# Performance work log

Hardware: AMD Instinct MI355X
Metric: run time of the kernel (lower is better)

## Reference

```python
import math
import jax, jax.numpy as jnp
import numpy as np

DIM = 256; DEPTH = 5; FANOUT = 10; VOCAB = 257
B = 16; T = 2048
NEXP = 8; HID = 512; TOPK = 2; TEMP = 1.0; HEADS = 2
CAPACITY = math.ceil(B * TOPK / NEXP * 1.1)  # capacity-based dispatch, =5
LAYER_SIZES = [FANOUT ** l for l in range(DEPTH)]  # [1,10,100,1000,10000]


def setup_inputs() -> dict:
    key = jax.random.key(0)
    ks = iter(jax.random.split(key, 64))
    def p(shape, scale=0.02):
        return jax.random.normal(next(ks), shape, jnp.float32) * scale
    inp = {
        'tokens': jax.random.randint(next(ks), (B, T), 0, VOCAB),
        'embed': p((VOCAB, DIM)),
        'pin_w': p((DIM, DIM)), 'pin_b': jnp.zeros(DIM, jnp.float32),
        'pch_w': p((DIM, DIM)), 'pch_b': jnp.zeros(DIM, jnp.float32),
        'depth_bias': p((DEPTH, DIM)),
        'q_w': p((DIM, DIM)), 'q_b': jnp.zeros(DIM, jnp.float32),
        'k_w': p((DIM, DIM)), 'k_b': jnp.zeros(DIM, jnp.float32),
        'v_w': p((DIM, DIM)), 'v_b': jnp.zeros(DIM, jnp.float32),
        'o_w': p((DIM, DIM)), 'o_b': jnp.zeros(DIM, jnp.float32),
        'level_gate': jnp.zeros(DEPTH, jnp.float32),
        'depth_gate': jnp.zeros((DEPTH, DIM), jnp.float32),
        'in_proj_w': p((DIM, 3 * DIM)), 'in_proj_b': jnp.zeros(3 * DIM, jnp.float32),
        'out_proj_w': p((DIM, DIM)), 'out_proj_b': jnp.zeros(DIM, jnp.float32),
        'ln_g': jnp.ones(DIM, jnp.float32), 'ln_b': jnp.zeros(DIM, jnp.float32),
        'ic_gate': jnp.zeros(1, jnp.float32),
        'gate_w': p((DIM, NEXP)), 'gate_b': jnp.zeros(NEXP, jnp.float32),
        'ew1': p((NEXP, DIM, HID)), 'eb1': jnp.zeros((NEXP, HID), jnp.float32),
        'ew2': p((NEXP, HID, DIM)), 'eb2': jnp.zeros((NEXP, DIM), jnp.float32),
        'hw1': p((DIM, DIM)), 'hb1': jnp.zeros(DIM, jnp.float32),
        'hw2': p((DIM, VOCAB)), 'hb2': jnp.zeros(VOCAB, jnp.float32),
    }
    return inp


def _fractal(context, pin_w, pin_b, pch_w, pch_b, depth_bias, q_w, q_b, k_w, k_b,
             v_w, v_b, o_w, o_b, level_gate, depth_gate,
             in_proj_w, in_proj_b, out_proj_w, out_proj_b, ln_g, ln_b, ic_gate):
    Bc = context.shape[0]
    base = context @ pin_w + pin_b                       # [B,D]
    y_next = None
    level_means = [None] * DEPTH
    inv_sqrt_d = 1.0 / math.sqrt(DIM)
    for l in reversed(range(DEPTH)):
        n = LAYER_SIZES[l]
        if l == DEPTH - 1:
            child_agg = jnp.zeros((Bc, n, DIM), context.dtype)
        else:
            yg = y_next.reshape(Bc, n, FANOUT, DIM)      # children grouped per parent
            q = (base + depth_bias[l]) @ q_w + q_b       # [B,D], shared across nodes
            k = yg @ k_w + k_b
            v = yg @ v_w + v_b
            att = jax.nn.softmax(jnp.einsum('bd,bnfd->bnf', q, k) * inv_sqrt_d, axis=-1)
            child_agg = jax.nn.sigmoid(depth_gate[l]) * jnp.einsum('bnf,bnfd->bnd', att, v)
        gate = jax.nn.sigmoid(level_gate[l])
        upd = (base[:, None, :] + depth_bias[l][None, None, :] + child_agg @ pch_w + pch_b) * gate
        y = jax.nn.relu(upd) @ o_w + o_b                 # [B,n,D]
        level_means[l] = y.mean(axis=1)
        y_next = y
    root = y_next[:, 0, :]                               # n==1 at level 0
    # interconnect: MHA over per-level means [B,DEPTH,D]
    z = jnp.stack(level_means, axis=1)
    qkv = z @ in_proj_w + in_proj_b
    qh, kh, vh = jnp.split(qkv, 3, axis=-1)
    hd = DIM // HEADS
    def to_heads(t):
        return t.reshape(Bc, DEPTH, HEADS, hd).transpose(0, 2, 1, 3)
    qh, kh, vh = to_heads(qh), to_heads(kh), to_heads(vh)
    aw = jax.nn.softmax(jnp.einsum('bhqd,bhkd->bhqk', qh, kh) / math.sqrt(hd), axis=-1)
    z2 = jnp.einsum('bhqk,bhkd->bhqd', aw, vh).transpose(0, 2, 1, 3).reshape(Bc, DEPTH, DIM)
    z2 = z2 @ out_proj_w + out_proj_b
    zs = z + z2
    mu = zs.mean(-1, keepdims=True)
    var = ((zs - mu) ** 2).mean(-1, keepdims=True)
    zn = (zs - mu) / jnp.sqrt(var + 1e-5) * ln_g + ln_b
    return root + jax.nn.sigmoid(ic_gate) * zn[:, 0, :]


def _moe(ctx, gate_w, gate_b, ew1, eb1, ew2, eb2):
    scaled = (ctx @ gate_w + gate_b) / TEMP
    top_vals, top_idx = jax.lax.top_k(scaled, TOPK)      # [B,K]
    gs = jax.nn.softmax(top_vals, axis=-1)               # [B,K], strictly > 0
    out = jnp.zeros_like(ctx)
    for e in range(NEXP):                                # fixed small expert loop
        sflat = jnp.where(top_idx == e, gs, -1.0).reshape(-1)   # [B*K]
        vals, pos = jax.lax.top_k(sflat, CAPACITY)       # capacity-limited dispatch
        w = jnp.where(vals > 0.0, vals, 0.0)             # drop unassigned/overflow
        tok = pos // TOPK
        xin = ctx[tok]                                   # [cap,D]
        eo = jax.nn.relu(xin @ ew1[e] + eb1[e]) @ ew2[e] + eb2[e]
        out = out.at[tok].add(eo * w[:, None])
    return out


def reference(tokens, embed, pin_w, pin_b, pch_w, pch_b, depth_bias,
              q_w, q_b, k_w, k_b, v_w, v_b, o_w, o_b, level_gate, depth_gate,
              in_proj_w, in_proj_b, out_proj_w, out_proj_b, ln_g, ln_b, ic_gate,
              gate_w, gate_b, ew1, eb1, ew2, eb2, hw1, hb1, hw2, hb2):
    x = embed[tokens]                                    # [B,T,D]
    context = x.mean(axis=1)                             # [B,D]
    root = _fractal(context, pin_w, pin_b, pch_w, pch_b, depth_bias, q_w, q_b,
                    k_w, k_b, v_w, v_b, o_w, o_b, level_gate, depth_gate,
                    in_proj_w, in_proj_b, out_proj_w, out_proj_b, ln_g, ln_b, ic_gate)
    root = root + _moe(root, gate_w, gate_b, ew1, eb1, ew2, eb2)
    h = x + root[:, None, :]                             # per-token logits from context + token emb
    logits = jax.nn.relu(h @ hw1 + hb1) @ hw2 + hb2      # [B,T,V]
    return logits
```

## Files before the change

### kernel.cpp

```cpp
#include <hip/hip_runtime.h>
#include <hip/hip_bf16.h>
#include <math.h>

#define DIM    256
#define DEPTH  5
#define FANOUT 10
#define VOCAB  257
#define BB     16
#define TT     2048
#define NEXP   8
#define HID    512
#define TOPK   2
#define CAP    5

__device__ __forceinline__ float sigm(float x) { return 1.f / (1.f + expf(-x)); }

__device__ __forceinline__ void mv8x2(const float* sv, const float* __restrict__ W,
                                      int kseg, int cq, float red[16][DIM]) {
  const float* Wp = W + (size_t)kseg * 16 * DIM + cq * 4;
  float4 acc = {0.f, 0.f, 0.f, 0.f};
#pragma unroll 1
  for (int h = 0; h < 2; ++h) {
    float4 wv[8];
#pragma unroll
    for (int i = 0; i < 8; ++i)
      wv[i] = *(const float4*)(Wp + (size_t)(h * 8 + i) * DIM);
#pragma unroll
    for (int i = 0; i < 8; ++i) {
      float s = sv[kseg * 16 + h * 8 + i];
      acc.x = fmaf(s, wv[i].x, acc.x);
      acc.y = fmaf(s, wv[i].y, acc.y);
      acc.z = fmaf(s, wv[i].z, acc.z);
      acc.w = fmaf(s, wv[i].w, acc.w);
    }
    __builtin_amdgcn_sched_barrier(0);
  }
  *(float4*)&red[kseg][cq * 4] = acc;
}

__device__ __forceinline__ float sum16(const float red[16][DIM], int d) {
  float s = 0.f;
#pragma unroll
  for (int g = 0; g < 16; ++g) s += red[g][d];
  return s;
}

__global__ void __launch_bounds__(1024) k_fractal(
    const int* __restrict__ tokens, const float* __restrict__ embed,
    const float* __restrict__ pin_w, const float* __restrict__ pin_b,
    const float* __restrict__ pch_w, const float* __restrict__ pch_b,
    const float* __restrict__ depth_bias,
    const float* __restrict__ v_w, const float* __restrict__ v_b,
    const float* __restrict__ o_w, const float* __restrict__ o_b,
    const float* __restrict__ level_gate, const float* __restrict__ depth_gate,
    const float* __restrict__ in_proj_w, const float* __restrict__ in_proj_b,
    const float* __restrict__ out_proj_w, const float* __restrict__ out_proj_b,
    const float* __restrict__ ln_g, const float* __restrict__ ln_b,
    const float* __restrict__ ic_gate,
    float* __restrict__ rootA, float* __restrict__ root2,
    int* __restrict__ bidx, int* __restrict__ boff) {
  int b = blockIdx.x;
  int tid = threadIdx.x;
  int d = tid & 255;
  int ks = tid >> 8;
  int k0 = ks * 64;
  int kseg = tid >> 6;
  int cq = tid & 63;
  __shared__ int cnt[VOCAB];
  __shared__ float sv[DIM];
  __shared__ float basev[DIM];
  __shared__ float ym[DEPTH][DIM];
  __shared__ float q0v[DIM], kh[DEPTH][DIM], vh[DEPTH][DIM];
  __shared__ float red11[4][11][DIM];
  __shared__ float zsv[DIM];
  __shared__ float aw[16];
  __shared__ float redl[8];
  __shared__ int offb[VOCAB + 1];
  __shared__ int woff[VOCAB];
  float (*red16)[DIM] = reinterpret_cast<float(*)[DIM]>(&red11[0][0][0]);

  for (int i = tid; i < VOCAB; i += 1024) cnt[i] = 0;
  __syncthreads();
  for (int t = tid; t < TT; t += 1024) atomicAdd(&cnt[tokens[b * TT + t]], 1);
  __syncthreads();
  {
    const float* Ep = embed + (size_t)kseg * 16 * DIM + cq * 4;
    float4 acc = {0.f, 0.f, 0.f, 0.f};
#pragma unroll 1
    for (int h = 0; h < 2; ++h) {
      float4 ev[8];
#pragma unroll
      for (int i = 0; i < 8; ++i)
        ev[i] = *(const float4*)(Ep + (size_t)(h * 8 + i) * DIM);
#pragma unroll
      for (int i = 0; i < 8; ++i) {
        float cv = (float)cnt[kseg * 16 + h * 8 + i];
        acc.x = fmaf(cv, ev[i].x, acc.x);
        acc.y = fmaf(cv, ev[i].y, acc.y);
        acc.z = fmaf(cv, ev[i].z, acc.z);
        acc.w = fmaf(cv, ev[i].w, acc.w);
      }
      __builtin_amdgcn_sched_barrier(0);
    }
    *(float4*)&red16[kseg][cq * 4] = acc;
  }
  __syncthreads();
  if (ks == 0) {
    float s = sum16(red16, d);
    s = fmaf((float)cnt[256], embed[(size_t)256 * DIM + d], s);
    sv[d] = s * (1.0f / (float)TT);
  }
  __syncthreads();

  mv8x2(sv, pin_w, kseg, cq, red16);
  __syncthreads();
  if (ks == 0) {
    float base = sum16(red16, d) + pin_b[d];
    basev[d] = base;
    float u = (base + depth_bias[4 * DIM + d] + pch_b[d]) * sigm(level_gate[4]);
    sv[d] = fmaxf(u, 0.f);
  }
  __syncthreads();
  mv8x2(sv, o_w, kseg, cq, red16);
  __syncthreads();
  if (ks == 0) {
    float y = sum16(red16, d) + o_b[d];
    ym[4][d] = y;
    sv[d] = y;
  }
  __syncthreads();
  for (int l = 3; l >= 0; --l) {
    mv8x2(sv, v_w, kseg, cq, red16);
    __syncthreads();
    if (ks == 0) {
      float vv = sum16(red16, d) + v_b[d];
      sv[d] = sigm(depth_gate[l * DIM + d]) * vv;
    }
    __syncthreads();
    mv8x2(sv, pch_w, kseg, cq, red16);
    __syncthreads();
    if (ks == 0) {
      float t = sum16(red16, d) + pch_b[d];
      float u = (basev[d] + depth_bias[l * DIM + d] + t) * sigm(level_gate[l]);
      sv[d] = fmaxf(u, 0.f);
    }
    __syncthreads();
    mv8x2(sv, o_w, kseg, cq, red16);
    __syncthreads();
    if (ks == 0) {
      float y = sum16(red16, d) + o_b[d];
      ym[l][d] = y;
      sv[d] = y;
    }
    __syncthreads();
  }
  {
    float aq = 0.f;
    float ak0 = 0.f, ak1 = 0.f, ak2 = 0.f, ak3 = 0.f, ak4 = 0.f;
    float av0 = 0.f, av1 = 0.f, av2 = 0.f, av3 = 0.f, av4 = 0.f;
#pragma unroll
    for (int h = 0; h < 8; ++h) {
      int kb = k0 + h * 8;
      float wq[8], wk[8], wv8[8];
#pragma unroll
      for (int i = 0; i < 8; ++i) {
        const float* wrow = in_proj_w + (size_t)(kb + i) * 768;
        wq[i] = wrow[d]; wk[i] = wrow[256 + d]; wv8[i] = wrow[512 + d];
      }
#pragma unroll
      for (int i = 0; i < 8; ++i) {
        float z0 = ym[0][kb + i];
        aq  = fmaf(z0, wq[i], aq);
        ak0 = fmaf(z0, wk[i], ak0);
        av0 = fmaf(z0, wv8[i], av0);
        float z1 = ym[1][kb + i];
        ak1 = fmaf(z1, wk[i], ak1);
        av1 = fmaf(z1, wv8[i], av1);
        float z2 = ym[2][kb + i];
        ak2 = fmaf(z2, wk[i], ak2);
        av2 = fmaf(z2, wv8[i], av2);
        float z3 = ym[3][kb + i];
        ak3 = fmaf(z3, wk[i], ak3);
        av3 = fmaf(z3, wv8[i], av3);
        float z4 = ym[4][kb + i];
        ak4 = fmaf(z4, wk[i], ak4);
        av4 = fmaf(z4, wv8[i], av4);
      }
    }
    red11[ks][0][d] = ak0; red11[ks][1][d] = ak1; red11[ks][2][d] = ak2;
    red11[ks][3][d] = ak3; red11[ks][4][d] = ak4;
    red11[ks][5][d] = av0; red11[ks][6][d] = av1; red11[ks][7][d] = av2;
    red11[ks][8][d] = av3; red11[ks][9][d] = av4;
    red11[ks][10][d] = aq;
  }
  __syncthreads();
  for (int idx = tid; idx < 11 * DIM; idx += 1024) {
    int c = idx >> 8, dd = idx & 255;
    float sum = red11[0][c][dd] + red11[1][c][dd] + red11[2][c][dd] + red11[3][c][dd];
    if (c < 5)       kh[c][dd]     = sum + in_proj_b[256 + dd];
    else if (c < 10) vh[c - 5][dd] = sum + in_proj_b[512 + dd];
    else             q0v[dd]       = sum + in_proj_b[dd];
  }
  __syncthreads();
  {
    int wid = tid >> 6;
    if (wid < 10) {
      int h = wid / 5, l = wid - h * 5;
      int lane = tid & 63;
      float s = q0v[h * 128 + lane] * kh[l][h * 128 + lane];
      s = fmaf(q0v[h * 128 + 64 + lane], kh[l][h * 128 + 64 + lane], s);
      for (int o = 32; o > 0; o >>= 1) s += __shfl_down(s, o, 64);
      if (lane == 0) aw[wid] = s * 0.08838834764831845f;
    }
  }
  __syncthreads();
  if (tid < 2) {
    float m = aw[tid * 5];
    for (int l = 1; l < 5; ++l) m = fmaxf(m, aw[tid * 5 + l]);
    float e[5], ssum = 0.f;
    for (int l = 0; l < 5; ++l) { e[l] = expf(aw[tid * 5 + l] - m); ssum += e[l]; }
    for (int l = 0; l < 5; ++l) aw[tid * 5 + l] = e[l] / ssum;
  }
  __syncthreads();
  if (ks == 0) {
    int h = d >> 7;
    float z2 = 0.f;
    for (int l = 0; l < 5; ++l) z2 = fmaf(aw[h * 5 + l], vh[l][d], z2);
    sv[d] = z2;
  }
  __syncthreads();
  mv8x2(sv, out_proj_w, kseg, cq, red16);
  __syncthreads();
  if (ks == 0) {
    float z2p = sum16(red16, d) + out_proj_b[d];
    zsv[d] = ym[0][d] + z2p;
  }
  __syncthreads();
  float zs = 0.f, df = 0.f, mu = 0.f;
  if (tid < 256) {
    zs = zsv[tid];
    float v = zs;
    for (int o = 32; o > 0; o >>= 1) v += __shfl_down(v, o, 64);
    if ((tid & 63) == 0) redl[tid >> 6] = v;
  }
  __syncthreads();
  if (tid < 256) {
    mu = (redl[0] + redl[1] + redl[2] + redl[3]) * (1.f / 256.f);
    df = zs - mu;
  }
  __syncthreads();
  if (tid < 256) {
    float v = df * df;
    for (int o = 32; o > 0; o >>= 1) v += __shfl_down(v, o, 64);
    if ((tid & 63) == 0) redl[tid >> 6] = v;
  }
  __syncthreads();
  if (tid < 256) {
    float var = (redl[0] + redl[1] + redl[2] + redl[3]) * (1.f / 256.f);
    float zn = df / sqrtf(var + 1e-5f) * ln_g[tid] + ln_b[tid];
    float r = ym[0][tid] + sigm(ic_gate[0]) * zn;
    rootA[b * DIM + tid] = r;
    root2[b * DIM + tid] = r;
  }
  __syncthreads();
  if (tid == 0) {
    int a = 0;
    for (int v = 0; v < VOCAB; ++v) { offb[v] = a; a += cnt[v]; }
    offb[VOCAB] = a;
  }
  __syncthreads();
  if (tid <= VOCAB) boff[b * (VOCAB + 1) + tid] = offb[tid];
  if (tid < VOCAB) woff[tid] = offb[tid];
  __syncthreads();
  for (int t = tid; t < TT; t += 1024) {
    int tok = tokens[b * TT + t];
    int p = atomicAdd(&woff[tok], 1);
    bidx[b * TT + p] = t;
  }
}

__global__ void __launch_bounds__(256) k_expert1(
    const float* __restrict__ rootA,
    const float* __restrict__ gate_w, const float* __restrict__ gate_b,
    const float* __restrict__ ew1, const float* __restrict__ eb1,
    int* __restrict__ etok, float* __restrict__ ewt,
    float* __restrict__ hid_ws) {
  int bx = blockIdx.x;
  int e = bx >> 3, jt = bx & 7, j0 = jt * 64;
  int tid = threadIdx.x, w = tid >> 6, lane = tid & 63;
  __shared__ float xin[CAP][DIM];
  __shared__ float red[CAP][4][64];
  __shared__ float sc[BB * NEXP];
  __shared__ float gs[BB * TOPK];
  __shared__ int gidx[BB * TOPK];
  __shared__ int stok[CAP];
  __shared__ float swt[CAP];
  if (tid < BB * NEXP) {
    int b = tid >> 3, ep = tid & 7;
    float chunk[8];
#pragma unroll
    for (int g = 0; g < 8; ++g) {
      float acc = 0.f;
#pragma unroll 8
      for (int i = 0; i < 32; ++i) {
        int k = g * 32 + i;
        acc = fmaf(rootA[b * DIM + k], gate_w[k * NEXP + ep], acc);
      }
      chunk[g] = acc;
    }
    float s = gate_b[ep];
#pragma unroll
    for (int g = 0; g < 8; ++g) s += chunk[g];
    sc[tid] = s;
  }
  __syncthreads();
  if (tid < BB) {
    int bb = tid;
    int i0 = 0; float v0 = sc[bb * 8 + 0];
    for (int ee = 1; ee < 8; ++ee) { float v = sc[bb * 8 + ee]; if (v > v0) { v0 = v; i0 = ee; } }
    int i1 = -1; float v1 = -1e30f;
    for (int ee = 0; ee < 8; ++ee) {
      if (ee == i0) continue;
      float v = sc[bb * 8 + ee];
      if (v > v1) { v1 = v; i1 = ee; }
    }
    float e1v = expf(v1 - v0);
    float s = 1.f + e1v;
    gs[bb * 2 + 0] = 1.f / s;  gidx[bb * 2 + 0] = i0;
    gs[bb * 2 + 1] = e1v / s;  gidx[bb * 2 + 1] = i1;
  }
  __syncthreads();
  if (tid == 0) {
    unsigned used = 0u;
    for (int s = 0; s < CAP; ++s) {
      int bi = 0; float bv = -1e30f;
      for (int i = 0; i < 32; ++i) {
        if (used & (1u << i)) continue;
        float v = (gidx[i] == e) ? gs[i] : -1.0f;
        if (v > bv) { bv = v; bi = i; }
      }
      used |= (1u << bi);
      stok[s] = bi >> 1;
      swt[s] = bv > 0.f ? bv : 0.f;
    }
  }
  __syncthreads();
  if (jt == 0 && tid < CAP) {
    etok[e * CAP + tid] = stok[tid];
    ewt[e * CAP + tid] = swt[tid];
  }
  for (int idx = tid; idx < CAP * DIM; idx += 256) {
    int s = idx >> 8, k = idx & 255;
    xin[s][k] = rootA[stok[s] * DIM + k];
  }
  __syncthreads();
  float a0 = 0.f, a1 = 0.f, a2 = 0.f, a3 = 0.f, a4 = 0.f;
  const float* W = ew1 + (size_t)e * DIM * HID + j0 + lane;
  int kbase = w * 64;
#pragma unroll
  for (int h = 0; h < 8; ++h) {
    float wv[8];
#pragma unroll
    for (int i = 0; i < 8; ++i) wv[i] = W[(size_t)(kbase + h * 8 + i) * HID];
#pragma unroll
    for (int i = 0; i < 8; ++i) {
      int k = kbase + h * 8 + i;
      a0 = fmaf(xin[0][k], wv[i], a0);
      a1 = fmaf(xin[1][k], wv[i], a1);
      a2 = fmaf(xin[2][k], wv[i], a2);
      a3 = fmaf(xin[3][k], wv[i], a3);
      a4 = fmaf(xin[4][k], wv[i], a4);
    }
  }
  red[0][w][lane] = a0; red[1][w][lane] = a1; red[2][w][lane] = a2;
  red[3][w][lane] = a3; red[4][w][lane] = a4;
  __syncthreads();
  for (int idx = tid; idx < CAP * 64; idx += 256) {
    int s = idx >> 6, j = idx & 63;
    float sum = red[s][0][j] + red[s][1][j] + red[s][2][j] + red[s][3][j]
              + eb1[e * HID + j0 + j];
    hid_ws[((size_t)(e * CAP + s)) * HID + j0 + j] = fmaxf(sum, 0.f);
  }
}

__global__ void __launch_bounds__(256) k_expert2(
    const float* __restrict__ hid_ws,
    const float* __restrict__ ew2, const float* __restrict__ eb2,
    const float* __restrict__ ewt, const int* __restrict__ etok,
    float* __restrict__ root2) {
  int bx = blockIdx.x;
  int e = bx >> 3, dt = bx & 7, d0 = dt * 32;
  int tid = threadIdx.x, seg = tid >> 5, c = tid & 31;
  __shared__ float hv[CAP][HID];
  __shared__ float red[CAP][8][32];
  for (int idx = tid; idx < CAP * HID; idx += 256) {
    int s = idx >> 9, k = idx & 511;
    hv[s][k] = hid_ws[((size_t)(e * CAP + s)) * HID + k];
  }
  __syncthreads();
  float a0 = 0.f, a1 = 0.f, a2 = 0.f, a3 = 0.f, a4 = 0.f;
  const float* W = ew2 + (size_t)e * HID * DIM + d0 + c;
  int kbase = seg * 64;
#pragma unroll
  for (int h = 0; h < 8; ++h) {
    float wv[8];
#pragma unroll
    for (int i = 0; i < 8; ++i) wv[i] = W[(size_t)(kbase + h * 8 + i) * DIM];
#pragma unroll
    for (int i = 0; i < 8; ++i) {
      int k = kbase + h * 8 + i;
      a0 = fmaf(hv[0][k], wv[i], a0);
      a1 = fmaf(hv[1][k], wv[i], a1);
      a2 = fmaf(hv[2][k], wv[i], a2);
      a3 = fmaf(hv[3][k], wv[i], a3);
      a4 = fmaf(hv[4][k], wv[i], a4);
    }
  }
  red[0][seg][c] = a0; red[1][seg][c] = a1; red[2][seg][c] = a2;
  red[3][seg][c] = a3; red[4][seg][c] = a4;
  __syncthreads();
  if (tid < CAP * 32) {
    int s = tid >> 5, cc = tid & 31;
    float sum = 0.f;
#pragma unroll
    for (int g = 0; g < 8; ++g) sum += red[s][g][cc];
    sum += eb2[e * DIM + d0 + cc];
    float w = ewt[e * CAP + s];
    if (w > 0.f)
      atomicAdd(&root2[etok[e * CAP + s] * DIM + d0 + cc], sum * w);
  }
}

__global__ void __launch_bounds__(256) k_logits(
    const float* __restrict__ embed, const float* __restrict__ root2,
    const float* __restrict__ hw1, const float* __restrict__ hb1,
    const float* __restrict__ hw2, const float* __restrict__ hb2,
    const int* __restrict__ bidx, const int* __restrict__ boff,
    float* __restrict__ out) {
  int tok = blockIdx.x, r0 = blockIdx.y * 4;
  int c = threadIdx.x;
  __shared__ float hrow[4][DIM];
  __shared__ float hid[4][DIM];
  __shared__ float tailred[4][17];
  __shared__ float tailv[4];
  {
    float ev = embed[(size_t)tok * DIM + c];
#pragma unroll
    for (int j = 0; j < 4; ++j) hrow[j][c] = ev + root2[(size_t)(r0 + j) * DIM + c];
  }
  __syncthreads();
  {
    float a0 = hb1[c], a1 = a0, a2 = a0, a3 = a0;
    for (int kb = 0; kb < DIM; kb += 8) {
      float wv[8];
#pragma unroll
      for (int i = 0; i < 8; ++i) wv[i] = hw1[(size_t)(kb + i) * DIM + c];
#pragma unroll
      for (int i = 0; i < 8; ++i) {
        int k = kb + i;
        a0 = fmaf(hrow[0][k], wv[i], a0);
        a1 = fmaf(hrow[1][k], wv[i], a1);
        a2 = fmaf(hrow[2][k], wv[i], a2);
        a3 = fmaf(hrow[3][k], wv[i], a3);
      }
    }
    hid[0][c] = fmaxf(a0, 0.f); hid[1][c] = fmaxf(a1, 0.f);
    hid[2][c] = fmaxf(a2, 0.f); hid[3][c] = fmaxf(a3, 0.f);
  }
  __syncthreads();
  float a0, a1, a2, a3;
  {
    a0 = hb2[c]; a1 = a0; a2 = a0; a3 = a0;
    for (int kb = 0; kb < DIM; kb += 8) {
      float wv[8];
#pragma unroll
      for (int i = 0; i < 8; ++i) wv[i] = hw2[(size_t)(kb + i) * VOCAB + c];
#pragma unroll
      for (int i = 0; i < 8; ++i) {
        int k = kb + i;
        a0 = fmaf(hid[0][k], wv[i], a0);
        a1 = fmaf(hid[1][k], wv[i], a1);
        a2 = fmaf(hid[2][k], wv[i], a2);
        a3 = fmaf(hid[3][k], wv[i], a3);
      }
    }
  }
  if (c < 64) {
    int r = c >> 4, seg = c & 15;
    float sum = 0.f;
#pragma unroll 4
    for (int i = 0; i < 16; ++i) {
      int k = seg * 16 + i;
      sum = fmaf(hid[r][k], hw2[(size_t)k * VOCAB + 256], sum);
    }
    tailred[r][seg] = sum;
  }
  __syncthreads();
  if (c < 4) {
    float a = hb2[256];
#pragma unroll
    for (int s = 0; s < 16; ++s) a += tailred[c][s];
    tailv[c] = a;
  }
  __syncthreads();
#pragma unroll
  for (int j = 0; j < 4; ++j) {
    int b = r0 + j;
    int s = boff[b * (VOCAB + 1) + tok];
    int e = boff[b * (VOCAB + 1) + tok + 1];
    float aj = (j == 0) ? a0 : (j == 1) ? a1 : (j == 2) ? a2 : a3;
    float tl = tailv[j];
    for (int m = s; m < e; ++m) {
      int t = bidx[b * TT + m];
      size_t base = (size_t)(b * TT + t) * VOCAB;
      out[base + c] = aj;
      if (c == 0) out[base + 256] = tl;
    }
  }
}

extern "C" void kernel_launch(void* const* d_in, const int* in_sizes, int n_in,
                              void* d_out, int out_size, void* d_ws, size_t ws_size,
                              hipStream_t stream) {
  (void)in_sizes; (void)n_in; (void)out_size; (void)ws_size;
  const int*   tokens     = (const int*)d_in[0];
  const float* embed      = (const float*)d_in[1];
  const float* pin_w      = (const float*)d_in[2];
  const float* pin_b      = (const float*)d_in[3];
  const float* pch_w      = (const float*)d_in[4];
  const float* pch_b      = (const float*)d_in[5];
  const float* depth_bias = (const float*)d_in[6];
  const float* v_w        = (const float*)d_in[11];
  const float* v_b        = (const float*)d_in[12];
  const float* o_w        = (const float*)d_in[13];
  const float* o_b        = (const float*)d_in[14];
  const float* level_gate = (const float*)d_in[15];
  const float* depth_gate = (const float*)d_in[16];
  const float* in_proj_w  = (const float*)d_in[17];
  const float* in_proj_b  = (const float*)d_in[18];
  const float* out_proj_w = (const float*)d_in[19];
  const float* out_proj_b = (const float*)d_in[20];
  const float* ln_g       = (const float*)d_in[21];
  const float* ln_b       = (const float*)d_in[22];
  const float* ic_gate    = (const float*)d_in[23];
  const float* gate_w     = (const float*)d_in[24];
  const float* gate_b     = (const float*)d_in[25];
  const float* ew1        = (const float*)d_in[26];
  const float* eb1        = (const float*)d_in[27];
  const float* ew2        = (const float*)d_in[28];
  const float* eb2        = (const float*)d_in[29];
  const float* hw1        = (const float*)d_in[30];
  const float* hb1        = (const float*)d_in[31];
  const float* hw2        = (const float*)d_in[32];
  const float* hb2        = (const float*)d_in[33];
  float* out = (float*)d_out;

  float* ws      = (float*)d_ws;
  float* rootA   = ws + 4096;
  float* root2   = ws + 8192;
  int*   etok    = (int*)(ws + 22528);
  float* ewt     = ws + 22576;
  float* hid_ws  = ws + 22656;
  int*   bidx    = (int*)(ws + 43136);
  int*   boff    = (int*)(ws + 75904);

  k_fractal<<<BB, 1024, 0, stream>>>(tokens, embed, pin_w, pin_b, pch_w, pch_b,
                                     depth_bias, v_w, v_b, o_w, o_b, level_gate,
                                     depth_gate, in_proj_w, in_proj_b, out_proj_w,
                                     out_proj_b, ln_g, ln_b, ic_gate, rootA, root2,
                                     bidx, boff);
  k_expert1<<<NEXP * 8, 256, 0, stream>>>(rootA, gate_w, gate_b, ew1, eb1,
                                          etok, ewt, hid_ws);
  k_expert2<<<NEXP * 8, 256, 0, stream>>>(hid_ws, ew2, eb2, ewt, etok, root2);
  k_logits<<<dim3(VOCAB, 4), 256, 0, stream>>>(embed, root2, hw1, hb1, hw2, hb2,
                                               bidx, boff, out);
}
```

Measured before the change: 253.2 us.

## Process all batches per vocab block in logits and stage gating inputs in LDS

After: 396.8 us. +56.7%, slower.

```diff
diff --git a/kernel.cpp b/kernel.cpp
--- a/kernel.cpp
+++ b/kernel.cpp
@@ -288,6 +288,8 @@
   int bx = blockIdx.x;
   int e = bx >> 3, jt = bx & 7, j0 = jt * 64;
   int tid = threadIdx.x, w = tid >> 6, lane = tid & 63;
+  __shared__ float rlds[BB * DIM];
+  __shared__ float gwlds[DIM * NEXP];
   __shared__ float xin[CAP][DIM];
   __shared__ float red[CAP][4][64];
   __shared__ float sc[BB * NEXP];
@@ -295,6 +297,11 @@
   __shared__ int gidx[BB * TOPK];
   __shared__ int stok[CAP];
   __shared__ float swt[CAP];
+  for (int idx = tid; idx < BB * DIM / 4; idx += 256)
+    *(float4*)&rlds[idx * 4] = *(const float4*)&rootA[idx * 4];
+  for (int idx = tid; idx < DIM * NEXP / 4; idx += 256)
+    *(float4*)&gwlds[idx * 4] = *(const float4*)&gate_w[idx * 4];
+  __syncthreads();
   if (tid < BB * NEXP) {
     int b = tid >> 3, ep = tid & 7;
     float chunk[8];
@@ -304,7 +311,7 @@
 #pragma unroll 8
       for (int i = 0; i < 32; ++i) {
         int k = g * 32 + i;
-        acc = fmaf(rootA[b * DIM + k], gate_w[k * NEXP + ep], acc);
+        acc = fmaf(rlds[b * DIM + k], gwlds[k * NEXP + ep], acc);
       }
       chunk[g] = acc;
     }
@@ -351,7 +358,7 @@
   }
   for (int idx = tid; idx < CAP * DIM; idx += 256) {
     int s = idx >> 8, k = idx & 255;
-    xin[s][k] = rootA[stok[s] * DIM + k];
+    xin[s][k] = rlds[stok[s] * DIM + k];
   }
   __syncthreads();
   float a0 = 0.f, a1 = 0.f, a2 = 0.f, a3 = 0.f, a4 = 0.f;
@@ -437,55 +444,87 @@
     const float* __restrict__ hw2, const float* __restrict__ hb2,
     const int* __restrict__ bidx, const int* __restrict__ boff,
     float* __restrict__ out) {
-  int tok = blockIdx.x, r0 = blockIdx.y * 4;
+  int tok = blockIdx.x;
   int c = threadIdx.x;
-  __shared__ float hrow[4][DIM];
-  __shared__ float hid[4][DIM];
-  __shared__ float tailred[4][17];
-  __shared__ float tailv[4];
+  __shared__ float hrow[BB][DIM];
+  __shared__ float wtile[64][DIM];
+  __shared__ float hid[BB][DIM];
+  __shared__ float tailred[BB][17];
+  __shared__ float tailv[BB];
+  __shared__ int tbuf[TT];
   {
     float ev = embed[(size_t)tok * DIM + c];
 #pragma unroll
-    for (int j = 0; j < 4; ++j) hrow[j][c] = ev + root2[(size_t)(r0 + j) * DIM + c];
-  }
-  __syncthreads();
+    for (int j = 0; j < BB; ++j) hrow[j][c] = ev + root2[(size_t)j * DIM + c];
+  }
+  float acc[BB];
+#pragma unroll
+  for (int r = 0; r < BB; ++r) acc[r] = hb1[c];
+#pragma unroll 1
+  for (int kt = 0; kt < 4; ++kt) {
+    __syncthreads();
+    for (int idx = c; idx < 64 * 64; idx += 256) {
+      int r = idx >> 6, c4 = idx & 63;
+      *(float4*)&wtile[r][c4 * 4] =
+          *(const float4*)&hw1[(size_t)(kt * 64 + r) * DIM + c4 * 4];
+    }
+    __syncthreads();
+#pragma unroll 1
+    for (int kb = 0; kb < 64; kb += 8) {
+      int kk = kt * 64 + kb;
+      float wv[8];
+#pragma unroll
+      for (int i = 0; i < 8; ++i) wv[i] = wtile[kb + i][c];
+#pragma unroll
+      for (int r = 0; r < BB; ++r) {
+        float4 h0 = *(const float4*)&hrow[r][kk];
+        float4 h1 = *(const float4*)&hrow[r][kk + 4];
+        acc[r] = fmaf(h0.x, wv[0], acc[r]);
+        acc[r] = fmaf(h0.y, wv[1], acc[r]);
+        acc[r] = fmaf(h0.z, wv[2], acc[r]);
+        acc[r] = fmaf(h0.w, wv[3], acc[r]);
+        acc[r] = fmaf(h1.x, wv[4], acc[r]);
+        acc[r] = fmaf(h1.y, wv[5], acc[r]);
+        acc[r] = fmaf(h1.z, wv[6], acc[r]);
+        acc[r] = fmaf(h1.w, wv[7], acc[r]);
+      }
+    }
+  }
+#pragma unroll
+  for (int r = 0; r < BB; ++r) hid[r][c] = fmaxf(acc[r], 0.f);
+  float acc2[BB];
+#pragma unroll
+  for (int r = 0; r < BB; ++r) acc2[r] = hb2[c];
+#pragma unroll 1
+  for (int kt = 0; kt < 4; ++kt) {
+    __syncthreads();
+    for (int idx = c; idx < 64 * 256; idx += 256) {
+      int r = idx >> 8, cc = idx & 255;
+      wtile[r][cc] = hw2[(size_t)(kt * 64 + r) * VOCAB + cc];
+    }
+    __syncthreads();
+#pragma unroll 1
+    for (int kb = 0; kb < 64; kb += 8) {
+      int kk = kt * 64 + kb;
+      float wv[8];
+#pragma unroll
+      for (int i = 0; i < 8; ++i) wv[i] = wtile[kb + i][c];
+#pragma unroll
+      for (int r = 0; r < BB; ++r) {
+        float4 h0 = *(const float4*)&hid[r][kk];
+        float4 h1 = *(const float4*)&hid[r][kk + 4];
+        acc2[r] = fmaf(h0.x, wv[0], acc2[r]);
+        acc2[r] = fmaf(h0.y, wv[1], acc2[r]);
+        acc2[r] = fmaf(h0.z, wv[2], acc2[r]);
+        acc2[r] = fmaf(h0.w, wv[3], acc2[r]);
+        acc2[r] = fmaf(h1.x, wv[4], acc2[r]);
+        acc2[r] = fmaf(h1.y, wv[5], acc2[r]);
+        acc2[r] = fmaf(h1.z, wv[6], acc2[r]);
+        acc2[r] = fmaf(h1.w, wv[7], acc2[r]);
+      }
+    }
+  }
   {
-    float a0 = hb1[c], a1 = a0, a2 = a0, a3 = a0;
-    for (int kb = 0; kb < DIM; kb += 8) {
-      float wv[8];
-#pragma unroll
-      for (int i = 0; i < 8; ++i) wv[i] = hw1[(size_t)(kb + i) * DIM + c];
-#pragma unroll
-      for (int i = 0; i < 8; ++i) {
-        int k = kb + i;
-        a0 = fmaf(hrow[0][k], wv[i], a0);
-        a1 = fmaf(hrow[1][k], wv[i], a1);
-        a2 = fmaf(hrow[2][k], wv[i], a2);
-        a3 = fmaf(hrow[3][k], wv[i], a3);
-      }
-    }
-    hid[0][c] = fmaxf(a0, 0.f); hid[1][c] = fmaxf(a1, 0.f);
-    hid[2][c] = fmaxf(a2, 0.f); hid[3][c] = fmaxf(a3, 0.f);
-  }
-  __syncthreads();
-  float a0, a1, a2, a3;
-  {
-    a0 = hb2[c]; a1 = a0; a2 = a0; a3 = a0;
-    for (int kb = 0; kb < DIM; kb += 8) {
-      float wv[8];
-#pragma unroll
-      for (int i = 0; i < 8; ++i) wv[i] = hw2[(size_t)(kb + i) * VOCAB + c];
-#pragma unroll
-      for (int i = 0; i < 8; ++i) {
-        int k = kb + i;
-        a0 = fmaf(hid[0][k], wv[i], a0);
-        a1 = fmaf(hid[1][k], wv[i], a1);
-        a2 = fmaf(hid[2][k], wv[i], a2);
-        a3 = fmaf(hid[3][k], wv[i], a3);
-      }
-    }
-  }
-  if (c < 64) {
     int r = c >> 4, seg = c & 15;
     float sum = 0.f;
 #pragma unroll 4
@@ -496,22 +535,28 @@
     tailred[r][seg] = sum;
   }
   __syncthreads();
-  if (c < 4) {
+  if (c < BB) {
     float a = hb2[256];
 #pragma unroll
     for (int s = 0; s < 16; ++s) a += tailred[c][s];
     tailv[c] = a;
   }
-  __syncthreads();
-#pragma unroll
-  for (int j = 0; j < 4; ++j) {
-    int b = r0 + j;
+#pragma unroll
+  for (int r = 0; r < BB; ++r) hid[r][c] = acc2[r];
+  __syncthreads();
+#pragma unroll 1
+  for (int b = 0; b < BB; ++b) {
     int s = boff[b * (VOCAB + 1) + tok];
     int e = boff[b * (VOCAB + 1) + tok + 1];
-    float aj = (j == 0) ? a0 : (j == 1) ? a1 : (j == 2) ? a2 : a3;
-    float tl = tailv[j];
-    for (int m = s; m < e; ++m) {
-      int t = bidx[b * TT + m];
+    int n = e - s;
+    __syncthreads();
+    for (int m = c; m < n; m += 256) tbuf[m] = bidx[b * TT + s + m];
+    __syncthreads();
+    float aj = hid[b][c];
+    float tl = tailv[b];
+#pragma unroll 1
+    for (int m = 0; m < n; ++m) {
+      int t = tbuf[m];
       size_t base = (size_t)(b * TT + t) * VOCAB;
       out[base + c] = aj;
       if (c == 0) out[base + 256] = tl;
@@ -572,6 +617,6 @@
   k_expert1<<<NEXP * 8, 256, 0, stream>>>(rootA, gate_w, gate_b, ew1, eb1,
                                           etok, ewt, hid_ws);
   k_expert2<<<NEXP * 8, 256, 0, stream>>>(hid_ws, ew2, eb2, ewt, etok, root2);
-  k_logits<<<dim3(VOCAB, 4), 256, 0, stream>>>(embed, root2, hw1, hb1, hw2, hb2,
-                                               bidx, boff, out);
+  k_logits<<<VOCAB, 256, 0, stream>>>(embed, root2, hw1, hb1, hw2, hb2,
+                                      bidx, boff, out);
 }
```

## Fuse MoE expert layers into one kernel with split-K atomic second layer

Applied to the files above, without the earlier changes.

After: 244.3 us. 1.04x faster.

```diff
diff --git a/kernel.cpp b/kernel.cpp
--- a/kernel.cpp
+++ b/kernel.cpp
@@ -279,22 +279,30 @@
   }
 }
 
-__global__ void __launch_bounds__(256) k_expert1(
+__global__ void __launch_bounds__(256) k_moe(
     const float* __restrict__ rootA,
     const float* __restrict__ gate_w, const float* __restrict__ gate_b,
     const float* __restrict__ ew1, const float* __restrict__ eb1,
-    int* __restrict__ etok, float* __restrict__ ewt,
-    float* __restrict__ hid_ws) {
+    const float* __restrict__ ew2, const float* __restrict__ eb2,
+    float* __restrict__ root2) {
   int bx = blockIdx.x;
   int e = bx >> 3, jt = bx & 7, j0 = jt * 64;
   int tid = threadIdx.x, w = tid >> 6, lane = tid & 63;
+  __shared__ float rlds[BB * DIM];
+  __shared__ float gwlds[DIM * NEXP];
   __shared__ float xin[CAP][DIM];
   __shared__ float red[CAP][4][64];
+  __shared__ float hloc[CAP][64];
   __shared__ float sc[BB * NEXP];
   __shared__ float gs[BB * TOPK];
   __shared__ int gidx[BB * TOPK];
   __shared__ int stok[CAP];
   __shared__ float swt[CAP];
+  for (int idx = tid; idx < BB * DIM / 4; idx += 256)
+    *(float4*)&rlds[idx * 4] = *(const float4*)&rootA[idx * 4];
+  for (int idx = tid; idx < DIM * NEXP / 4; idx += 256)
+    *(float4*)&gwlds[idx * 4] = *(const float4*)&gate_w[idx * 4];
+  __syncthreads();
   if (tid < BB * NEXP) {
     int b = tid >> 3, ep = tid & 7;
     float chunk[8];
@@ -304,7 +312,7 @@
 #pragma unroll 8
       for (int i = 0; i < 32; ++i) {
         int k = g * 32 + i;
-        acc = fmaf(rootA[b * DIM + k], gate_w[k * NEXP + ep], acc);
+        acc = fmaf(rlds[b * DIM + k], gwlds[k * NEXP + ep], acc);
       }
       chunk[g] = acc;
     }
@@ -345,89 +353,70 @@
     }
   }
   __syncthreads();
-  if (jt == 0 && tid < CAP) {
-    etok[e * CAP + tid] = stok[tid];
-    ewt[e * CAP + tid] = swt[tid];
-  }
   for (int idx = tid; idx < CAP * DIM; idx += 256) {
     int s = idx >> 8, k = idx & 255;
-    xin[s][k] = rootA[stok[s] * DIM + k];
-  }
-  __syncthreads();
-  float a0 = 0.f, a1 = 0.f, a2 = 0.f, a3 = 0.f, a4 = 0.f;
-  const float* W = ew1 + (size_t)e * DIM * HID + j0 + lane;
-  int kbase = w * 64;
-#pragma unroll
-  for (int h = 0; h < 8; ++h) {
-    float wv[8];
-#pragma unroll
-    for (int i = 0; i < 8; ++i) wv[i] = W[(size_t)(kbase + h * 8 + i) * HID];
-#pragma unroll
-    for (int i = 0; i < 8; ++i) {
-      int k = kbase + h * 8 + i;
-      a0 = fmaf(xin[0][k], wv[i], a0);
-      a1 = fmaf(xin[1][k], wv[i], a1);
-      a2 = fmaf(xin[2][k], wv[i], a2);
-      a3 = fmaf(xin[3][k], wv[i], a3);
-      a4 = fmaf(xin[4][k], wv[i], a4);
-    }
-  }
-  red[0][w][lane] = a0; red[1][w][lane] = a1; red[2][w][lane] = a2;
-  red[3][w][lane] = a3; red[4][w][lane] = a4;
+    xin[s][k] = rlds[stok[s] * DIM + k];
+  }
+  __syncthreads();
+  {
+    float a0 = 0.f, a1 = 0.f, a2 = 0.f, a3 = 0.f, a4 = 0.f;
+    const float* W = ew1 + (size_t)e * DIM * HID + j0 + lane;
+    int kbase = w * 64;
+#pragma unroll
+    for (int h = 0; h < 8; ++h) {
+      float wv[8];
+#pragma unroll
+      for (int i = 0; i < 8; ++i) wv[i] = W[(size_t)(kbase + h * 8 + i) * HID];
+#pragma unroll
+      for (int i = 0; i < 8; ++i) {
+        int k = kbase + h * 8 + i;
+        a0 = fmaf(xin[0][k], wv[i], a0);
+        a1 = fmaf(xin[1][k], wv[i], a1);
+        a2 = fmaf(xin[2][k], wv[i], a2);
+        a3 = fmaf(xin[3][k], wv[i], a3);
+        a4 = fmaf(xin[4][k], wv[i], a4);
+      }
+    }
+    red[0][w][lane] = a0; red[1][w][lane] = a1; red[2][w][lane] = a2;
+    red[3][w][lane] = a3; red[4][w][lane] = a4;
+  }
   __syncthreads();
   for (int idx = tid; idx < CAP * 64; idx += 256) {
     int s = idx >> 6, j = idx & 63;
     float sum = red[s][0][j] + red[s][1][j] + red[s][2][j] + red[s][3][j]
               + eb1[e * HID + j0 + j];
-    hid_ws[((size_t)(e * CAP + s)) * HID + j0 + j] = fmaxf(sum, 0.f);
-  }
-}
-
-__global__ void __launch_bounds__(256) k_expert2(
-    const float* __restrict__ hid_ws,
-    const float* __restrict__ ew2, const float* __restrict__ eb2,
-    const float* __restrict__ ewt, const int* __restrict__ etok,
-    float* __restrict__ root2) {
-  int bx = blockIdx.x;
-  int e = bx >> 3, dt = bx & 7, d0 = dt * 32;
-  int tid = threadIdx.x, seg = tid >> 5, c = tid & 31;
-  __shared__ float hv[CAP][HID];
-  __shared__ float red[CAP][8][32];
-  for (int idx = tid; idx < CAP * HID; idx += 256) {
-    int s = idx >> 9, k = idx & 511;
-    hv[s][k] = hid_ws[((size_t)(e * CAP + s)) * HID + k];
-  }
-  __syncthreads();
-  float a0 = 0.f, a1 = 0.f, a2 = 0.f, a3 = 0.f, a4 = 0.f;
-  const float* W = ew2 + (size_t)e * HID * DIM + d0 + c;
-  int kbase = seg * 64;
-#pragma unroll
-  for (int h = 0; h < 8; ++h) {
-    float wv[8];
-#pragma unroll
-    for (int i = 0; i < 8; ++i) wv[i] = W[(size_t)(kbase + h * 8 + i) * DIM];
-#pragma unroll
-    for (int i = 0; i < 8; ++i) {
-      int k = kbase + h * 8 + i;
-      a0 = fmaf(hv[0][k], wv[i], a0);
-      a1 = fmaf(hv[1][k], wv[i], a1);
-      a2 = fmaf(hv[2][k], wv[i], a2);
-      a3 = fmaf(hv[3][k], wv[i], a3);
-      a4 = fmaf(hv[4][k], wv[i], a4);
-    }
-  }
-  red[0][seg][c] = a0; red[1][seg][c] = a1; red[2][seg][c] = a2;
-  red[3][seg][c] = a3; red[4][seg][c] = a4;
-  __syncthreads();
-  if (tid < CAP * 32) {
-    int s = tid >> 5, cc = tid & 31;
-    float sum = 0.f;
-#pragma unroll
-    for (int g = 0; g < 8; ++g) sum += red[s][g][cc];
-    sum += eb2[e * DIM + d0 + cc];
-    float w = ewt[e * CAP + s];
-    if (w > 0.f)
-      atomicAdd(&root2[etok[e * CAP + s] * DIM + d0 + cc], sum * w);
+    hloc[s][j] = fmaxf(sum, 0.f);
+  }
+  __syncthreads();
+  {
+    int d = tid;
+    float a0 = 0.f, a1 = 0.f, a2 = 0.f, a3 = 0.f, a4 = 0.f;
+    const float* W2 = ew2 + (size_t)e * HID * DIM + (size_t)j0 * DIM + d;
+#pragma unroll
+    for (int h = 0; h < 8; ++h) {
+      float wv[8];
+#pragma unroll
+      for (int i = 0; i < 8; ++i) wv[i] = W2[(size_t)(h * 8 + i) * DIM];
+#pragma unroll
+      for (int i = 0; i < 8; ++i) {
+        int j = h * 8 + i;
+        a0 = fmaf(hloc[0][j], wv[i], a0);
+        a1 = fmaf(hloc[1][j], wv[i], a1);
+        a2 = fmaf(hloc[2][j], wv[i], a2);
+        a3 = fmaf(hloc[3][j], wv[i], a3);
+        a4 = fmaf(hloc[4][j], wv[i], a4);
+      }
+    }
+    float bias = (jt == 0) ? eb2[e * DIM + d] : 0.f;
+    float pa[1];
+    (void)pa;
+#pragma unroll
+    for (int s = 0; s < CAP; ++s) {
+      float as = (s == 0) ? a0 : (s == 1) ? a1 : (s == 2) ? a2 : (s == 3) ? a3 : a4;
+      float wgt = swt[s];
+      if (wgt > 0.f)
+        atomicAdd(&root2[stok[s] * DIM + d], (as + bias) * wgt);
+    }
   }
 }
 
@@ -558,9 +547,6 @@
   float* ws      = (float*)d_ws;
   float* rootA   = ws + 4096;
   float* root2   = ws + 8192;
-  int*   etok    = (int*)(ws + 22528);
-  float* ewt     = ws + 22576;
-  float* hid_ws  = ws + 22656;
   int*   bidx    = (int*)(ws + 43136);
   int*   boff    = (int*)(ws + 75904);
 
@@ -569,9 +555,8 @@
                                      depth_gate, in_proj_w, in_proj_b, out_proj_w,
                                      out_proj_b, ln_g, ln_b, ic_gate, rootA, root2,
                                      bidx, boff);
-  k_expert1<<<NEXP * 8, 256, 0, stream>>>(rootA, gate_w, gate_b, ew1, eb1,
-                                          etok, ewt, hid_ws);
-  k_expert2<<<NEXP * 8, 256, 0, stream>>>(hid_ws, ew2, eb2, ewt, etok, root2);
+  k_moe<<<NEXP * 8, 256, 0, stream>>>(rootA, gate_w, gate_b, ew1, eb1,
+                                      ew2, eb2, root2);
   k_logits<<<dim3(VOCAB, 4), 256, 0, stream>>>(embed, root2, hw1, hb1, hw2, hb2,
                                                bidx, boff, out);
 }
```
